# Optimization experiments

Hardware: AMD Instinct MI355X
Metric: run time of the kernel (lower is better)

## Reference

```python
import jax, jax.numpy as jnp
import numpy as np

B, P, D = 128, 32, 256
DIST_THD = 1.5


def setup_inputs() -> dict:
    key = jax.random.key(0)
    ks = jax.random.split(key, 16)
    s2d = 1.0 / np.sqrt(2 * D)
    s1d = 1.0 / np.sqrt(D)
    return {
        "fea_data": jax.random.normal(ks[0], (B, P, D), jnp.float32),
        "pos_data": jax.random.normal(ks[1], (B, P, 2), jnp.float32),
        # pair_encoder: Linear(2D->D), ReLU, (Dropout=id), Linear(D->D); weights stored [in,out]
        "pe_w1": jax.random.normal(ks[2], (2 * D, D), jnp.float32) * s2d,
        "pe_b1": jax.random.normal(ks[3], (D,), jnp.float32) * s2d,
        "pe_w2": jax.random.normal(ks[4], (D, D), jnp.float32) * s1d,
        "pe_b2": jax.random.normal(ks[5], (D,), jnp.float32) * s1d,
        # spatial_mixer: same structure
        "sm_w1": jax.random.normal(ks[6], (2 * D, D), jnp.float32) * s2d,
        "sm_b1": jax.random.normal(ks[7], (D,), jnp.float32) * s2d,
        "sm_w2": jax.random.normal(ks[8], (D, D), jnp.float32) * s1d,
        "sm_b2": jax.random.normal(ks[9], (D,), jnp.float32) * s1d,
        "diff_wts": jax.random.normal(ks[10], (P, D), jnp.float32),
        "diff_bias": jax.random.normal(ks[11], (P,), jnp.float32),
        "gconv_wt": jax.random.normal(ks[12], (2 * D, D), jnp.float32),
    }


def reference(fea_data, pos_data, pe_w1, pe_b1, pe_w2, pe_b2,
              sm_w1, sm_b1, sm_w2, sm_b2, diff_wts, diff_bias, gconv_wt):
    dtype = fea_data.dtype
    # --- spatial_interact ---
    # pair_encoder(cat(x_p1, x_p2)): split W1 into the x_p1 and x_p2 halves so the
    # [B,P,P,2D] concat is never materialized.
    a = fea_data @ pe_w1[:D]          # [B,P,D] contribution of p1
    c = fea_data @ pe_w1[D:]          # [B,P,D] contribution of p2
    h = jax.nn.relu(a[:, :, None, :] + c[:, None, :, :] + pe_b1)  # [B,P,P,D]
    # sum over p2 of (h @ W2 + b2) == (sum h) @ W2 + P*b2 (linear)
    interact_sum = h.sum(axis=2) @ pe_w2 + P * pe_b2              # [B,P,D]
    mix_in = jnp.concatenate([fea_data, interact_sum], axis=-1)   # [B,P,2D]
    spatial = jax.nn.relu(mix_in @ sm_w1 + sm_b1) @ sm_w2 + sm_b2 # [B,P,D]
    # --- residual_diffs ---
    logits = fea_data @ diff_wts.T + diff_bias                    # [B,P(p1),P(p2)]
    w = jax.nn.softmax(logits, axis=-1)
    # sum_p2 w*(x_p1 - x_p2) = x_p1 - w @ x   (softmax weights sum to 1)
    diff = fea_data - jnp.einsum('bpq,bqd->bpd', w, fea_data)     # [B,P,D]
    merged = jnp.concatenate([spatial, diff], axis=-1)            # [B,P,2D]
    # --- neighbor_mat ---
    dist = jnp.linalg.norm(pos_data[:, :, None, :] - pos_data[:, None, :, :], axis=-1)
    off_diag = ~jnp.eye(P, dtype=bool)
    adj = ((dist < DIST_THD) & off_diag).astype(dtype)            # [B,P,P]
    # --- sync_gconv ---
    adj = adj + jnp.eye(P, dtype=dtype)
    deg = adj.sum(axis=2, keepdims=True) + 1e-6                   # [B,P,1]
    dinv = deg ** -0.5
    norm_adj = dinv * adj * jnp.swapaxes(dinv, 1, 2)
    out = jnp.einsum('bpq,bqf->bpf', norm_adj, merged) @ gconv_wt # [B,P,D]
    return jax.nn.relu(out)
```

## Files before the change

### kernel.cpp

```cpp
#include <hip/hip_runtime.h>
#include <math.h>

#define Dk 256
#define Pk 32
#define Bk 128

using f32x4    = __attribute__((ext_vector_type(4))) float;
using short8   = __attribute__((ext_vector_type(8))) short;
using short4v  = __attribute__((ext_vector_type(4))) short;
using ushort4v = __attribute__((ext_vector_type(4))) unsigned short;

static __device__ __forceinline__ unsigned short bf16_rtne(float x) {
    unsigned u = __float_as_uint(x);
    return (unsigned short)((u + 0x7fffu + ((u >> 16) & 1u)) >> 16);
}
static __device__ __forceinline__ float bf16_back(unsigned short h) {
    return __uint_as_float(((unsigned)h) << 16);
}
static __device__ __forceinline__ void split2(float x, unsigned short& h, unsigned short& l) {
    h = bf16_rtne(x);
    l = bf16_rtne(x - bf16_back(h));
}

__device__ __forceinline__ void gemm_core(
    const unsigned short* __restrict__ AH, const unsigned short* __restrict__ AL, int lda,
    const unsigned short* __restrict__ BloH, const unsigned short* __restrict__ BloL,
    const unsigned short* __restrict__ BhiH, const unsigned short* __restrict__ BhiL,
    int splitK, int K, int row0, int col0,
    short (*Ah)[72], short (*Al)[72], short (*Bh)[72], short (*Bl)[72],
    f32x4 acc[2][2])
{
    const int tid  = threadIdx.x;
    const int l    = tid & 63;
    const int w    = tid >> 6;
    const int wm   = w >> 1, wn = w & 1;
    const int role = l & 15, g = l >> 4;
    const int sr   = tid >> 3;
    const int scg  = (tid & 7) * 8;

    short8 pAH[2], pAL[2], pBH[2], pBL[2];
    auto prefetch = [&](int k0) {
        const unsigned short *bH, *bL; int kk;
        if (k0 < splitK) { bH = BloH; bL = BloL; kk = k0; }
        else             { bH = BhiH; bL = BhiL; kk = k0 - splitK; }
        #pragma unroll
        for (int it = 0; it < 2; ++it) {
            int r = sr + it * 32;
            pAH[it] = *(const short8*)(AH + (size_t)(row0 + r) * lda + k0 + scg);
            pAL[it] = *(const short8*)(AL + (size_t)(row0 + r) * lda + k0 + scg);
            pBH[it] = *(const short8*)(bH + (size_t)(col0 + r) * 256 + kk + scg);
            pBL[it] = *(const short8*)(bL + (size_t)(col0 + r) * 256 + kk + scg);
        }
    };

    prefetch(0);
    const int nk = K >> 6;
    for (int kt = 0; kt < nk; ++kt) {
        #pragma unroll
        for (int it = 0; it < 2; ++it) {
            int r = sr + it * 32;
            *(short8*)&Ah[r][scg] = pAH[it];
            *(short8*)&Al[r][scg] = pAL[it];
            *(short8*)&Bh[r][scg] = pBH[it];
            *(short8*)&Bl[r][scg] = pBL[it];
        }
        __syncthreads();
        if (kt + 1 < nk) prefetch((kt + 1) << 6);
        #pragma unroll
        for (int ks = 0; ks < 2; ++ks) {
            short8 fah[2], fal[2], fbh[2], fbl[2];
            #pragma unroll
            for (int mt = 0; mt < 2; ++mt) {
                int r = wm * 32 + mt * 16 + role, c = ks * 32 + g * 8;
                fah[mt] = *(const short8*)&Ah[r][c];
                fal[mt] = *(const short8*)&Al[r][c];
            }
            #pragma unroll
            for (int nt = 0; nt < 2; ++nt) {
                int r = wn * 32 + nt * 16 + role, c = ks * 32 + g * 8;
                fbh[nt] = *(const short8*)&Bh[r][c];
                fbl[nt] = *(const short8*)&Bl[r][c];
            }
            #pragma unroll
            for (int mt = 0; mt < 2; ++mt)
                #pragma unroll
                for (int nt = 0; nt < 2; ++nt) {
                    acc[mt][nt] = __builtin_amdgcn_mfma_f32_16x16x32_bf16(fah[mt], fbh[nt], acc[mt][nt], 0, 0, 0);
                    acc[mt][nt] = __builtin_amdgcn_mfma_f32_16x16x32_bf16(fah[mt], fbl[nt], acc[mt][nt], 0, 0, 0);
                    acc[mt][nt] = __builtin_amdgcn_mfma_f32_16x16x32_bf16(fal[mt], fbh[nt], acc[mt][nt], 0, 0, 0);
                }
        }
        __syncthreads();
    }
}

__global__ __launch_bounds__(256)
void prep_kernel(const float* __restrict__ fea, const float* __restrict__ pe_w1,
                 const float* __restrict__ pe_w2, const float* __restrict__ pe_b2,
                 const float* __restrict__ sm_w1, const float* __restrict__ sm_b1,
                 const float* __restrict__ sm_w2, const float* __restrict__ sm_b2,
                 const float* __restrict__ gconv,
                 const float* __restrict__ diff_wts, const float* __restrict__ diff_bias,
                 unsigned short* __restrict__ MIX2H, unsigned short* __restrict__ MIX2L,
                 unsigned short* __restrict__ WpTH,  unsigned short* __restrict__ WpTL,
                 unsigned short* __restrict__ SW1TH, unsigned short* __restrict__ SW1TL,
                 unsigned short* __restrict__ GBTH,  unsigned short* __restrict__ GBTL,
                 unsigned short* __restrict__ W1pTH, unsigned short* __restrict__ W1pTL,
                 unsigned short* __restrict__ W2pTH, unsigned short* __restrict__ W2pTL,
                 float* __restrict__ b1p, float* __restrict__ b2p,
                 unsigned short* __restrict__ CATH, unsigned short* __restrict__ CATL)
{
    __shared__ __align__(16) char smbuf[70272];
    const int blk = blockIdx.x;
    const int tid = threadIdx.x;

    if (blk < 256) {
        int r0 = blk * 16;
        #pragma unroll
        for (int i = 0; i < 4; ++i) {
            int q  = tid + i * 256;
            int r  = r0 + (q >> 6);
            int c4 = (q & 63) * 4;
            f32x4 v = *(const f32x4*)(fea + (size_t)r * 256 + c4);
            ushort4v h, lo;
            #pragma unroll
            for (int j = 0; j < 4; ++j) { unsigned short hh, ll; split2(v[j], hh, ll); h[j] = hh; lo[j] = ll; }
            *(ushort4v*)&MIX2H[(size_t)r * 512 + c4] = h;
            *(ushort4v*)&MIX2L[(size_t)r * 512 + c4] = lo;
        }
    } else if (blk < 320) {
        int t  = blk - 256;
        int grp = t >> 4, tt = t & 15;
        int tr = tt >> 2, tc = tt & 3;
        const float* src; unsigned short *dH, *dL; int ilv, ofs;
        if (grp == 0)      { src = pe_w1;         dH = WpTH;  dL = WpTL;  ilv = 1; ofs = 0; }
        else if (grp == 1) { src = pe_w1 + 65536; dH = WpTH;  dL = WpTL;  ilv = 1; ofs = 1; }
        else if (grp == 2) { src = sm_w1;         dH = SW1TH; dL = SW1TL; ilv = 0; ofs = 0; }
        else               { src = gconv + 65536; dH = GBTH;  dL = GBTL;  ilv = 0; ofs = 0; }
        float (*ts)[65] = (float (*)[65])smbuf;
        #pragma unroll
        for (int i = 0; i < 4; ++i) {
            int q = tid + i * 256;
            int r = q >> 4, c4 = (q & 15) * 4;
            f32x4 v = *(const f32x4*)(src + (size_t)(tr * 64 + r) * 256 + tc * 64 + c4);
            ts[r][c4 + 0] = v[0]; ts[r][c4 + 1] = v[1]; ts[r][c4 + 2] = v[2]; ts[r][c4 + 3] = v[3];
        }
        __syncthreads();
        #pragma unroll
        for (int i = 0; i < 4; ++i) {
            int q = tid + i * 256;
            int n = q >> 4, k4 = (q & 15) * 4;
            ushort4v h, lo;
            #pragma unroll
            for (int j = 0; j < 4; ++j) { unsigned short hh, ll; split2(ts[k4 + j][n], hh, ll); h[j] = hh; lo[j] = ll; }
            int srcN   = tc * 64 + n;
            int dstRow = ilv ? (2 * srcN + ofs) : srcN;
            *(ushort4v*)&dH[(size_t)dstRow * 256 + tr * 64 + k4] = h;
            *(ushort4v*)&dL[(size_t)dstRow * 256 + tr * 64 + k4] = lo;
        }
    } else if (blk < 322) {
        int j = tid;
        if (blk == 320) {
            float s = 0.f;
            for (int k = 0; k < 256; ++k) s = fmaf(pe_b2[k], sm_w1[(size_t)(256 + k) * 256 + j], s);
            b1p[j] = s * (float)Pk + sm_b1[j];
        } else {
            float s = 0.f;
            for (int k = 0; k < 256; ++k) s = fmaf(sm_b2[k], gconv[(size_t)k * 256 + j], s);
            b2p[j] = s;
        }
    } else if (blk < 354) {
        int u = blk - 322;
        int z = u >> 4, tt = u & 15;
        int row0 = (tt >> 2) * 64, col0 = (tt & 3) * 64;
        const float* Af; const float* Bf; unsigned short *dH, *dL;
        if (z == 0) { Af = pe_w2; Bf = sm_w1 + 65536; dH = W1pTH; dL = W1pTL; }
        else        { Af = sm_w2; Bf = gconv;         dH = W2pTH; dL = W2pTL; }
        short (*Ah)[72] = (short (*)[72])(smbuf);
        short (*Al)[72] = (short (*)[72])(smbuf + 9216);
        short (*Bh)[72] = (short (*)[72])(smbuf + 18432);
        short (*Bl)[72] = (short (*)[72])(smbuf + 27648);
        const int l = tid & 63, w = tid >> 6, wm = w >> 1, wn = w & 1, role = l & 15, g = l >> 4;
        const int ar = tid >> 2, ac = (tid & 3) << 4;
        const int bc = (tid & 15) << 2, bk = (tid >> 4) << 2;
        f32x4 acc[2][2];
        #pragma unroll
        for (int i = 0; i < 2; ++i)
            #pragma unroll
            for (int j = 0; j < 2; ++j) acc[i][j] = (f32x4){0.f, 0.f, 0.f, 0.f};
        f32x4 aPf[4], bPf[4];
        auto load_tile = [&](int k0) {
            const float* Ap = Af + (size_t)(row0 + ar) * 256 + k0 + ac;
            #pragma unroll
            for (int j = 0; j < 4; ++j) aPf[j] = *(const f32x4*)(Ap + j * 4);
            #pragma unroll
            for (int jj = 0; jj < 4; ++jj)
                bPf[jj] = *(const f32x4*)(Bf + (size_t)(k0 + bk + jj) * 256 + col0 + bc);
        };
        load_tile(0);
        for (int kt = 0; kt < 4; ++kt) {
            {
                short8 h0, h1, l0, l1;
                #pragma unroll
                for (int j = 0; j < 4; ++j)
                    #pragma unroll
                    for (int e = 0; e < 4; ++e) {
                        unsigned short hh, ll; split2(aPf[j][e], hh, ll);
                        int idx = j * 4 + e;
                        if (idx < 8) { h0[idx] = (short)hh; l0[idx] = (short)ll; }
                        else         { h1[idx - 8] = (short)hh; l1[idx - 8] = (short)ll; }
                    }
                *(short8*)&Ah[ar][ac] = h0; *(short8*)&Ah[ar][ac + 8] = h1;
                *(short8*)&Al[ar][ac] = l0; *(short8*)&Al[ar][ac + 8] = l1;
                #pragma unroll
                for (int j = 0; j < 4; ++j) {
                    short4v h4, l4;
                    #pragma unroll
                    for (int jj = 0; jj < 4; ++jj) {
                        unsigned short hh, ll; split2(bPf[jj][j], hh, ll);
                        h4[jj] = (short)hh; l4[jj] = (short)ll;
                    }
                    *(short4v*)&Bh[bc + j][bk] = h4;
                    *(short4v*)&Bl[bc + j][bk] = l4;
                }
            }
            __syncthreads();
            if (kt + 1 < 4) load_tile((kt + 1) << 6);
            #pragma unroll
            for (int ks = 0; ks < 2; ++ks) {
                short8 fah[2], fal[2], fbh[2], fbl[2];
                #pragma unroll
                for (int mt = 0; mt < 2; ++mt) {
                    int r = wm * 32 + mt * 16 + role, c = ks * 32 + g * 8;
                    fah[mt] = *(const short8*)&Ah[r][c];
                    fal[mt] = *(const short8*)&Al[r][c];
                }
                #pragma unroll
                for (int nt = 0; nt < 2; ++nt) {
                    int r = wn * 32 + nt * 16 + role, c = ks * 32 + g * 8;
                    fbh[nt] = *(const short8*)&Bh[r][c];
                    fbl[nt] = *(const short8*)&Bl[r][c];
                }
                #pragma unroll
                for (int mt = 0; mt < 2; ++mt)
                    #pragma unroll
                    for (int nt = 0; nt < 2; ++nt) {
                        acc[mt][nt] = __builtin_amdgcn_mfma_f32_16x16x32_bf16(fah[mt], fbh[nt], acc[mt][nt], 0, 0, 0);
                        acc[mt][nt] = __builtin_amdgcn_mfma_f32_16x16x32_bf16(fah[mt], fbl[nt], acc[mt][nt], 0, 0, 0);
                        acc[mt][nt] = __builtin_amdgcn_mfma_f32_16x16x32_bf16(fal[mt], fbh[nt], acc[mt][nt], 0, 0, 0);
                    }
            }
            __syncthreads();
        }
        #pragma unroll
        for (int mt = 0; mt < 2; ++mt)
            #pragma unroll
            for (int nt = 0; nt < 2; ++nt) {
                int col = col0 + wn * 32 + nt * 16 + role;
                #pragma unroll
                for (int r = 0; r < 4; ++r) {
                    int row = row0 + wm * 32 + mt * 16 + g * 4 + r;
                    unsigned short hh, ll; split2(acc[mt][nt][r], hh, ll);
                    dH[(size_t)col * 256 + row] = hh;
                    dL[(size_t)col * 256 + row] = ll;
                }
            }
    } else {
        int b = blk - 354;
        float (*fs)[260] = (float (*)[260])(smbuf);
        float (*dwT)[32] = (float (*)[32])(smbuf + 33280);
        float (*wm_)[33] = (float (*)[33])(smbuf + 66048);
        const float* fb = fea + (size_t)b * 8192;
        #pragma unroll
        for (int i = 0; i < 8; ++i) {
            int q = tid + i * 256;
            int r = q >> 6, c4 = (q & 63) << 2;
            f32x4 v = *(const f32x4*)(fb + r * 256 + c4);
            fs[r][c4 + 0] = v[0]; fs[r][c4 + 1] = v[1]; fs[r][c4 + 2] = v[2]; fs[r][c4 + 3] = v[3];
        }
        {
            int p2 = tid & 31, kq = tid >> 5;
            #pragma unroll
            for (int i = 0; i < 8; ++i) {
                int c4 = ((kq << 3) + i) << 2;
                f32x4 v = *(const f32x4*)(diff_wts + (size_t)p2 * 256 + c4);
                dwT[c4 + 0][p2] = v[0]; dwT[c4 + 1][p2] = v[1];
                dwT[c4 + 2][p2] = v[2]; dwT[c4 + 3][p2] = v[3];
            }
        }
        __syncthreads();
        {
            const int p1 = tid >> 3, p2b = (tid & 7) << 2;
            f32x4 s = {0.f, 0.f, 0.f, 0.f};
            for (int k4 = 0; k4 < 256; k4 += 4) {
                f32x4 fv = *(const f32x4*)&fs[p1][k4];
                #pragma unroll
                for (int e = 0; e < 4; ++e) {
                    f32x4 dv = *(const f32x4*)&dwT[k4 + e][p2b];
                    s[0] = fmaf(fv[e], dv[0], s[0]);
                    s[1] = fmaf(fv[e], dv[1], s[1]);
                    s[2] = fmaf(fv[e], dv[2], s[2]);
                    s[3] = fmaf(fv[e], dv[3], s[3]);
                }
            }
            #pragma unroll
            for (int j = 0; j < 4; ++j) wm_[p1][p2b + j] = s[j] + diff_bias[p2b + j];
        }
        __syncthreads();
        if (tid < 32) {
            float m = wm_[tid][0];
            #pragma unroll
            for (int j = 1; j < 32; ++j) m = fmaxf(m, wm_[tid][j]);
            float e[32]; float sum = 0.f;
            #pragma unroll
            for (int j = 0; j < 32; ++j) { e[j] = __expf(wm_[tid][j] - m); sum += e[j]; }
            float inv = 1.f / sum;
            #pragma unroll
            for (int j = 0; j < 32; ++j) wm_[tid][j] = e[j] * inv;
        }
        __syncthreads();
        float fv[32];
        #pragma unroll
        for (int p2 = 0; p2 < 32; ++p2) fv[p2] = fs[p2][tid];
        for (int p1 = 0; p1 < 32; ++p1) {
            float s = 0.f;
            #pragma unroll
            for (int p2 = 0; p2 < 32; ++p2) s = fmaf(wm_[p1][p2], fv[p2], s);
            float v = fv[p1] - s;
            unsigned short hh, ll; split2(v, hh, ll);
            size_t o = (size_t)(b * 32 + p1) * 512 + 256 + tid;
            CATH[o] = hh; CATL[o] = ll;
        }
    }
}

__global__ __launch_bounds__(256)
void g1_hsum(const unsigned short* __restrict__ MIX2H, const unsigned short* __restrict__ MIX2L,
             const unsigned short* __restrict__ WpTH, const unsigned short* __restrict__ WpTL,
             const float* __restrict__ pe_b1,
             unsigned short* __restrict__ MH, unsigned short* __restrict__ ML)
{
    __shared__ __align__(16) char smbuf[36864];
    short (*Ah)[72] = (short (*)[72])(smbuf);
    short (*Al)[72] = (short (*)[72])(smbuf + 9216);
    short (*Bh)[72] = (short (*)[72])(smbuf + 18432);
    short (*Bl)[72] = (short (*)[72])(smbuf + 27648);
    const int row0 = blockIdx.y * 64, col0 = blockIdx.x * 64;
    f32x4 acc[2][2];
    #pragma unroll
    for (int i = 0; i < 2; ++i)
        #pragma unroll
        for (int j = 0; j < 2; ++j) acc[i][j] = (f32x4){0.f, 0.f, 0.f, 0.f};

    gemm_core(MIX2H, MIX2L, 512, WpTH, WpTL, nullptr, nullptr, 1 << 30, 256,
              row0, col0, Ah, Al, Bh, Bl, acc);

    float (*ms)[68] = (float (*)[68])(smbuf);
    const int tid = threadIdx.x;
    const int l = tid & 63, w = tid >> 6, wm = w >> 1, wn = w & 1, role = l & 15, g = l >> 4;
    #pragma unroll
    for (int mt = 0; mt < 2; ++mt)
        #pragma unroll
        for (int nt = 0; nt < 2; ++nt)
            #pragma unroll
            for (int r = 0; r < 4; ++r)
                ms[wm * 32 + mt * 16 + g * 4 + r][wn * 32 + nt * 16 + role] = acc[mt][nt][r];
    __syncthreads();

    const int dd = tid & 31, bloc = (tid >> 5) & 1, pg = tid >> 6;
    const float b1v = pe_b1[blockIdx.x * 32 + dd];
    float apre[8], sum[8];
    #pragma unroll
    for (int i = 0; i < 8; ++i) {
        apre[i] = ms[bloc * 32 + pg * 8 + i][2 * dd] + b1v;
        sum[i] = 0.f;
    }
    for (int p2 = 0; p2 < 32; ++p2) {
        float cv = ms[bloc * 32 + p2][2 * dd + 1];
        #pragma unroll
        for (int i = 0; i < 8; ++i) sum[i] += fmaxf(apre[i] + cv, 0.f);
    }
    const int colg = 256 + blockIdx.x * 32 + dd;
    #pragma unroll
    for (int i = 0; i < 8; ++i) {
        int rowg = (2 * blockIdx.y + bloc) * 32 + pg * 8 + i;
        unsigned short hh, ll; split2(sum[i], hh, ll);
        MH[(size_t)rowg * 512 + colg] = hh;
        ML[(size_t)rowg * 512 + colg] = ll;
    }
}

__global__ __launch_bounds__(256)
void g3_kernel(const unsigned short* __restrict__ MIX2H, const unsigned short* __restrict__ MIX2L,
               const unsigned short* __restrict__ SW1TH, const unsigned short* __restrict__ SW1TL,
               const unsigned short* __restrict__ W1pTH, const unsigned short* __restrict__ W1pTL,
               const float* __restrict__ b1p,
               unsigned short* __restrict__ CATH, unsigned short* __restrict__ CATL)
{
    __shared__ __align__(16) char smbuf[36864];
    short (*Ah)[72] = (short (*)[72])(smbuf);
    short (*Al)[72] = (short (*)[72])(smbuf + 9216);
    short (*Bh)[72] = (short (*)[72])(smbuf + 18432);
    short (*Bl)[72] = (short (*)[72])(smbuf + 27648);
    const int row0 = blockIdx.y * 64, col0 = blockIdx.x * 64;
    f32x4 acc[2][2];
    #pragma unroll
    for (int i = 0; i < 2; ++i)
        #pragma unroll
        for (int j = 0; j < 2; ++j) acc[i][j] = (f32x4){0.f, 0.f, 0.f, 0.f};

    gemm_core(MIX2H, MIX2L, 512, SW1TH, SW1TL, W1pTH, W1pTL, 256, 512,
              row0, col0, Ah, Al, Bh, Bl, acc);

    const int tid = threadIdx.x;
    const int l = tid & 63, w = tid >> 6, wm = w >> 1, wn = w & 1, role = l & 15, g = l >> 4;
    float bv[2];
    #pragma unroll
    for (int nt = 0; nt < 2; ++nt) bv[nt] = b1p[col0 + wn * 32 + nt * 16 + role];
    #pragma unroll
    for (int mt = 0; mt < 2; ++mt)
        #pragma unroll
        for (int nt = 0; nt < 2; ++nt) {
            int col = col0 + wn * 32 + nt * 16 + role;
            #pragma unroll
            for (int r = 0; r < 4; ++r) {
                int row = row0 + wm * 32 + mt * 16 + g * 4 + r;
                float v = fmaxf(acc[mt][nt][r] + bv[nt], 0.f);
                unsigned short hh, ll; split2(v, hh, ll);
                CATH[(size_t)row * 512 + col] = hh;
                CATL[(size_t)row * 512 + col] = ll;
            }
        }
}

__global__ __launch_bounds__(256)
void g5_adj(const unsigned short* __restrict__ CATH, const unsigned short* __restrict__ CATL,
            const unsigned short* __restrict__ W2pTH, const unsigned short* __restrict__ W2pTL,
            const unsigned short* __restrict__ GBTH, const unsigned short* __restrict__ GBTL,
            const float* __restrict__ b2p, const float* __restrict__ pos,
            float* __restrict__ out)
{
    __shared__ __align__(16) char smbuf[44032];
    short (*Ah)[72] = (short (*)[72])(smbuf);
    short (*Al)[72] = (short (*)[72])(smbuf + 9216);
    short (*Bh)[72] = (short (*)[72])(smbuf + 18432);
    short (*Bl)[72] = (short (*)[72])(smbuf + 27648);
    const int row0 = blockIdx.y * 64, col0 = blockIdx.x * 64;
    f32x4 acc[2][2];
    #pragma unroll
    for (int i = 0; i < 2; ++i)
        #pragma unroll
        for (int j = 0; j < 2; ++j) acc[i][j] = (f32x4){0.f, 0.f, 0.f, 0.f};

    gemm_core(CATH, CATL, 512, W2pTH, W2pTL, GBTH, GBTL, 256, 512,
              row0, col0, Ah, Al, Bh, Bl, acc);

    float (*ms)[68]  = (float (*)[68])(smbuf);
    float* px        = (float*)(smbuf + 17408);
    float* py        = (float*)(smbuf + 17664);
    float* dinv_     = (float*)(smbuf + 17920);
    float (*na)[33]  = (float (*)[33])(smbuf + 18176);
    float (*ot)[68]  = (float (*)[68])(smbuf + 26624);

    const int tid = threadIdx.x;
    const int l = tid & 63, w = tid >> 6, wm = w >> 1, wn = w & 1, role = l & 15, g = l >> 4;
    float bv[2];
    #pragma unroll
    for (int nt = 0; nt < 2; ++nt) bv[nt] = b2p[col0 + wn * 32 + nt * 16 + role];
    #pragma unroll
    for (int mt = 0; mt < 2; ++mt)
        #pragma unroll
        for (int nt = 0; nt < 2; ++nt)
            #pragma unroll
            for (int r = 0; r < 4; ++r)
                ms[wm * 32 + mt * 16 + g * 4 + r][wn * 32 + nt * 16 + role] = acc[mt][nt][r] + bv[nt];

    const int b0 = 2 * blockIdx.y;
    if (tid < 64) {
        int bi = tid >> 5, pp = tid & 31;
        px[bi * 32 + pp] = pos[(size_t)(b0 + bi) * 64 + pp * 2 + 0];
        py[bi * 32 + pp] = pos[(size_t)(b0 + bi) * 64 + pp * 2 + 1];
    }
    __syncthreads();
    {
        int bi = tid >> 7, p1 = (tid >> 2) & 31, p2g = (tid & 3) * 8;
        #pragma unroll
        for (int j = 0; j < 8; ++j) {
            int p2 = p2g + j;
            float v;
            if (p1 == p2) v = 1.f;
            else {
                float dx = px[bi * 32 + p1] - px[bi * 32 + p2];
                float dy = py[bi * 32 + p1] - py[bi * 32 + p2];
                v = (sqrtf(dx * dx + dy * dy) < 1.5f) ? 1.f : 0.f;
            }
            na[bi * 32 + p1][p2] = v;
        }
    }
    __syncthreads();
    if (tid < 64) {
        int r = tid;
        float s = 0.f;
        #pragma unroll
        for (int j = 0; j < 32; ++j) s += na[r][j];
        dinv_[r] = 1.f / sqrtf(s + 1e-6f);
    }
    __syncthreads();
    {
        int bi = tid >> 7, p1 = (tid >> 2) & 31, p2g = (tid & 3) * 8;
        #pragma unroll
        for (int j = 0; j < 8; ++j) {
            int p2 = p2g + j;
            na[bi * 32 + p1][p2] *= dinv_[bi * 32 + p1] * dinv_[bi * 32 + p2];
        }
    }
    __syncthreads();
    {
        const int p1 = tid & 31, bi = (tid >> 5) & 1, fg = (tid >> 6) * 16;
        f32x4 s4[4];
        #pragma unroll
        for (int j = 0; j < 4; ++j) s4[j] = (f32x4){0.f, 0.f, 0.f, 0.f};
        for (int p2 = 0; p2 < 32; ++p2) {
            float nv = na[bi * 32 + p1][p2];
            const f32x4* mrow = (const f32x4*)&ms[bi * 32 + p2][fg];
            #pragma unroll
            for (int j = 0; j < 4; ++j) {
                f32x4 mv = mrow[j];
                s4[j][0] = fmaf(nv, mv[0], s4[j][0]);
                s4[j][1] = fmaf(nv, mv[1], s4[j][1]);
                s4[j][2] = fmaf(nv, mv[2], s4[j][2]);
                s4[j][3] = fmaf(nv, mv[3], s4[j][3]);
            }
        }
        #pragma unroll
        for (int j = 0; j < 4; ++j)
            #pragma unroll
            for (int e = 0; e < 4; ++e)
                ot[bi * 32 + p1][fg + j * 4 + e] = s4[j][e];
    }
    __syncthreads();
    #pragma unroll
    for (int i = 0; i < 16; ++i) {
        int q = tid + i * 256;
        int row = q >> 6, f = q & 63;
        out[(size_t)(b0 * 32 + row) * 256 + col0 + f] = fmaxf(ot[row][f], 0.f);
    }
}

extern "C" void kernel_launch(void* const* d_in, const int* in_sizes, int n_in,
                              void* d_out, int out_size, void* d_ws, size_t ws_size,
                              hipStream_t stream)
{
    const float* fea       = (const float*)d_in[0];
    const float* pos       = (const float*)d_in[1];
    const float* pe_w1     = (const float*)d_in[2];
    const float* pe_b1     = (const float*)d_in[3];
    const float* pe_w2     = (const float*)d_in[4];
    const float* pe_b2     = (const float*)d_in[5];
    const float* sm_w1     = (const float*)d_in[6];
    const float* sm_b1     = (const float*)d_in[7];
    const float* sm_w2     = (const float*)d_in[8];
    const float* sm_b2     = (const float*)d_in[9];
    const float* diff_wts  = (const float*)d_in[10];
    const float* diff_bias = (const float*)d_in[11];
    const float* gconv     = (const float*)d_in[12];
    float* out = (float*)d_out;
    char*  ws  = (char*)d_ws;

    unsigned short* MIX2H = (unsigned short*)(ws + 0);
    unsigned short* MIX2L = (unsigned short*)(ws + 4194304);
    unsigned short* CATH  = (unsigned short*)(ws + 8388608);
    unsigned short* CATL  = (unsigned short*)(ws + 12582912);
    unsigned short* WpTH  = (unsigned short*)(ws + 16777216);
    unsigned short* WpTL  = (unsigned short*)(ws + 17039360);
    unsigned short* SW1TH = (unsigned short*)(ws + 17301504);
    unsigned short* SW1TL = (unsigned short*)(ws + 17432576);
    unsigned short* GBTH  = (unsigned short*)(ws + 17563648);
    unsigned short* GBTL  = (unsigned short*)(ws + 17694720);
    unsigned short* W1pTH = (unsigned short*)(ws + 17825792);
    unsigned short* W1pTL = (unsigned short*)(ws + 17956864);
    unsigned short* W2pTH = (unsigned short*)(ws + 18087936);
    unsigned short* W2pTL = (unsigned short*)(ws + 18219008);
    float*          b1p   = (float*)(ws + 18350080);
    float*          b2p   = (float*)(ws + 18351104);

    prep_kernel<<<482, 256, 0, stream>>>(fea, pe_w1, pe_w2, pe_b2, sm_w1, sm_b1,
                                         sm_w2, sm_b2, gconv, diff_wts, diff_bias,
                                         MIX2H, MIX2L, WpTH, WpTL, SW1TH, SW1TL,
                                         GBTH, GBTL, W1pTH, W1pTL, W2pTH, W2pTL,
                                         b1p, b2p, CATH, CATL);
    g1_hsum<<<dim3(8, 64), 256, 0, stream>>>(MIX2H, MIX2L, WpTH, WpTL, pe_b1, MIX2H, MIX2L);
    g3_kernel<<<dim3(4, 64), 256, 0, stream>>>(MIX2H, MIX2L, SW1TH, SW1TL, W1pTH, W1pTL,
                                               b1p, CATH, CATL);
    g5_adj<<<dim3(4, 64), 256, 0, stream>>>(CATH, CATL, W2pTH, W2pTL, GBTH, GBTL,
                                            b2p, pos, out);
}
```

Baseline: 128.6 us.

## Merge four kernel launches into one cooperative persistent kernel with grid syncs

Turns the prep, g1, g3 and g5 kernels into device functions and calls them from a single cooperative kernel of 256 blocks, with grid.sync() between stages. Blocks loop over the 482 prep roles and the 512 g1 tiles. The aim is to remove the launch gaps and per-kernel tail costs between the four stages. The trade-off is fewer blocks, which lowers parallelism for prep and g1, a larger shared-memory footprint for every stage, and the cost of each grid barrier. If the cooperative launch fails, it falls back to four launches.

```diff
diff --git a/kernel.cpp b/kernel.cpp
--- a/kernel.cpp
+++ b/kernel.cpp
@@ -1,5 +1,8 @@
 #include <hip/hip_runtime.h>
+#include <hip/hip_cooperative_groups.h>
 #include <math.h>
+
+namespace cg = cooperative_groups;
 
 #define Dk 256
 #define Pk 32
@@ -21,6 +24,16 @@
     h = bf16_rtne(x);
     l = bf16_rtne(x - bf16_back(h));
 }
+
+struct Args {
+    const float *fea, *pos, *pe_w1, *pe_b1, *pe_w2, *pe_b2;
+    const float *sm_w1, *sm_b1, *sm_w2, *sm_b2, *diff_wts, *diff_bias, *gconv;
+    unsigned short *MIX2H, *MIX2L, *WpTH, *WpTL, *SW1TH, *SW1TL, *GBTH, *GBTL;
+    unsigned short *W1pTH, *W1pTL, *W2pTH, *W2pTL;
+    float *b1p, *b2p;
+    unsigned short *CATH, *CATL;
+    float *out;
+};
 
 __device__ __forceinline__ void gemm_core(
     const unsigned short* __restrict__ AH, const unsigned short* __restrict__ AL, int lda,
@@ -94,26 +107,8 @@
     }
 }
 
-__global__ __launch_bounds__(256)
-void prep_kernel(const float* __restrict__ fea, const float* __restrict__ pe_w1,
-                 const float* __restrict__ pe_w2, const float* __restrict__ pe_b2,
-                 const float* __restrict__ sm_w1, const float* __restrict__ sm_b1,
-                 const float* __restrict__ sm_w2, const float* __restrict__ sm_b2,
-                 const float* __restrict__ gconv,
-                 const float* __restrict__ diff_wts, const float* __restrict__ diff_bias,
-                 unsigned short* __restrict__ MIX2H, unsigned short* __restrict__ MIX2L,
-                 unsigned short* __restrict__ WpTH,  unsigned short* __restrict__ WpTL,
-                 unsigned short* __restrict__ SW1TH, unsigned short* __restrict__ SW1TL,
-                 unsigned short* __restrict__ GBTH,  unsigned short* __restrict__ GBTL,
-                 unsigned short* __restrict__ W1pTH, unsigned short* __restrict__ W1pTL,
-                 unsigned short* __restrict__ W2pTH, unsigned short* __restrict__ W2pTL,
-                 float* __restrict__ b1p, float* __restrict__ b2p,
-                 unsigned short* __restrict__ CATH, unsigned short* __restrict__ CATL)
+__device__ __forceinline__ void do_role(const Args& A, char* smbuf, int blk, int tid)
 {
-    __shared__ __align__(16) char smbuf[70272];
-    const int blk = blockIdx.x;
-    const int tid = threadIdx.x;
-
     if (blk < 256) {
         int r0 = blk * 16;
         #pragma unroll
@@ -121,22 +116,22 @@
             int q  = tid + i * 256;
             int r  = r0 + (q >> 6);
             int c4 = (q & 63) * 4;
-            f32x4 v = *(const f32x4*)(fea + (size_t)r * 256 + c4);
+            f32x4 v = *(const f32x4*)(A.fea + (size_t)r * 256 + c4);
             ushort4v h, lo;
             #pragma unroll
             for (int j = 0; j < 4; ++j) { unsigned short hh, ll; split2(v[j], hh, ll); h[j] = hh; lo[j] = ll; }
-            *(ushort4v*)&MIX2H[(size_t)r * 512 + c4] = h;
-            *(ushort4v*)&MIX2L[(size_t)r * 512 + c4] = lo;
+            *(ushort4v*)&A.MIX2H[(size_t)r * 512 + c4] = h;
+            *(ushort4v*)&A.MIX2L[(size_t)r * 512 + c4] = lo;
         }
     } else if (blk < 320) {
         int t  = blk - 256;
         int grp = t >> 4, tt = t & 15;
         int tr = tt >> 2, tc = tt & 3;
         const float* src; unsigned short *dH, *dL; int ilv, ofs;
-        if (grp == 0)      { src = pe_w1;         dH = WpTH;  dL = WpTL;  ilv = 1; ofs = 0; }
-        else if (grp == 1) { src = pe_w1 + 65536; dH = WpTH;  dL = WpTL;  ilv = 1; ofs = 1; }
-        else if (grp == 2) { src = sm_w1;         dH = SW1TH; dL = SW1TL; ilv = 0; ofs = 0; }
-        else               { src = gconv + 65536; dH = GBTH;  dL = GBTL;  ilv = 0; ofs = 0; }
+        if (grp == 0)      { src = A.pe_w1;         dH = A.WpTH;  dL = A.WpTL;  ilv = 1; ofs = 0; }
+        else if (grp == 1) { src = A.pe_w1 + 65536; dH = A.WpTH;  dL = A.WpTL;  ilv = 1; ofs = 1; }
+        else if (grp == 2) { src = A.sm_w1;         dH = A.SW1TH; dL = A.SW1TL; ilv = 0; ofs = 0; }
+        else               { src = A.gconv + 65536; dH = A.GBTH;  dL = A.GBTL;  ilv = 0; ofs = 0; }
         float (*ts)[65] = (float (*)[65])smbuf;
         #pragma unroll
         for (int i = 0; i < 4; ++i) {
@@ -162,20 +157,20 @@
         int j = tid;
         if (blk == 320) {
             float s = 0.f;
-            for (int k = 0; k < 256; ++k) s = fmaf(pe_b2[k], sm_w1[(size_t)(256 + k) * 256 + j], s);
-            b1p[j] = s * (float)Pk + sm_b1[j];
+            for (int k = 0; k < 256; ++k) s = fmaf(A.pe_b2[k], A.sm_w1[(size_t)(256 + k) * 256 + j], s);
+            A.b1p[j] = s * (float)Pk + A.sm_b1[j];
         } else {
             float s = 0.f;
-            for (int k = 0; k < 256; ++k) s = fmaf(sm_b2[k], gconv[(size_t)k * 256 + j], s);
-            b2p[j] = s;
+            for (int k = 0; k < 256; ++k) s = fmaf(A.sm_b2[k], A.gconv[(size_t)k * 256 + j], s);
+            A.b2p[j] = s;
         }
     } else if (blk < 354) {
         int u = blk - 322;
         int z = u >> 4, tt = u & 15;
         int row0 = (tt >> 2) * 64, col0 = (tt & 3) * 64;
         const float* Af; const float* Bf; unsigned short *dH, *dL;
-        if (z == 0) { Af = pe_w2; Bf = sm_w1 + 65536; dH = W1pTH; dL = W1pTL; }
-        else        { Af = sm_w2; Bf = gconv;         dH = W2pTH; dL = W2pTL; }
+        if (z == 0) { Af = A.pe_w2; Bf = A.sm_w1 + 65536; dH = A.W1pTH; dL = A.W1pTL; }
+        else        { Af = A.sm_w2; Bf = A.gconv;         dH = A.W2pTH; dL = A.W2pTL; }
         short (*Ah)[72] = (short (*)[72])(smbuf);
         short (*Al)[72] = (short (*)[72])(smbuf + 9216);
         short (*Bh)[72] = (short (*)[72])(smbuf + 18432);
@@ -270,7 +265,7 @@
         float (*fs)[260] = (float (*)[260])(smbuf);
         float (*dwT)[32] = (float (*)[32])(smbuf + 33280);
         float (*wm_)[33] = (float (*)[33])(smbuf + 66048);
-        const float* fb = fea + (size_t)b * 8192;
+        const float* fb = A.fea + (size_t)b * 8192;
         #pragma unroll
         for (int i = 0; i < 8; ++i) {
             int q = tid + i * 256;
@@ -283,7 +278,7 @@
             #pragma unroll
             for (int i = 0; i < 8; ++i) {
                 int c4 = ((kq << 3) + i) << 2;
-                f32x4 v = *(const f32x4*)(diff_wts + (size_t)p2 * 256 + c4);
+                f32x4 v = *(const f32x4*)(A.diff_wts + (size_t)p2 * 256 + c4);
                 dwT[c4 + 0][p2] = v[0]; dwT[c4 + 1][p2] = v[1];
                 dwT[c4 + 2][p2] = v[2]; dwT[c4 + 3][p2] = v[3];
             }
@@ -304,7 +299,7 @@
                 }
             }
             #pragma unroll
-            for (int j = 0; j < 4; ++j) wm_[p1][p2b + j] = s[j] + diff_bias[p2b + j];
+            for (int j = 0; j < 4; ++j) wm_[p1][p2b + j] = s[j] + A.diff_bias[p2b + j];
         }
         __syncthreads();
         if (tid < 32) {
@@ -329,34 +324,29 @@
             float v = fv[p1] - s;
             unsigned short hh, ll; split2(v, hh, ll);
             size_t o = (size_t)(b * 32 + p1) * 512 + 256 + tid;
-            CATH[o] = hh; CATL[o] = ll;
-        }
-    }
-}
-
-__global__ __launch_bounds__(256)
-void g1_hsum(const unsigned short* __restrict__ MIX2H, const unsigned short* __restrict__ MIX2L,
-             const unsigned short* __restrict__ WpTH, const unsigned short* __restrict__ WpTL,
-             const float* __restrict__ pe_b1,
-             unsigned short* __restrict__ MH, unsigned short* __restrict__ ML)
+            A.CATH[o] = hh; A.CATL[o] = ll;
+        }
+    }
+}
+
+__device__ __forceinline__ void do_g1(const Args& A, char* smbuf, int t, int tid)
 {
-    __shared__ __align__(16) char smbuf[36864];
+    const int x = t & 7, y = t >> 3;
     short (*Ah)[72] = (short (*)[72])(smbuf);
     short (*Al)[72] = (short (*)[72])(smbuf + 9216);
     short (*Bh)[72] = (short (*)[72])(smbuf + 18432);
     short (*Bl)[72] = (short (*)[72])(smbuf + 27648);
-    const int row0 = blockIdx.y * 64, col0 = blockIdx.x * 64;
+    const int row0 = y * 64, col0 = x * 64;
     f32x4 acc[2][2];
     #pragma unroll
     for (int i = 0; i < 2; ++i)
         #pragma unroll
         for (int j = 0; j < 2; ++j) acc[i][j] = (f32x4){0.f, 0.f, 0.f, 0.f};
 
-    gemm_core(MIX2H, MIX2L, 512, WpTH, WpTL, nullptr, nullptr, 1 << 30, 256,
+    gemm_core(A.MIX2H, A.MIX2L, 512, A.WpTH, A.WpTL, nullptr, nullptr, 1 << 30, 256,
               row0, col0, Ah, Al, Bh, Bl, acc);
 
     float (*ms)[68] = (float (*)[68])(smbuf);
-    const int tid = threadIdx.x;
     const int l = tid & 63, w = tid >> 6, wm = w >> 1, wn = w & 1, role = l & 15, g = l >> 4;
     #pragma unroll
     for (int mt = 0; mt < 2; ++mt)
@@ -368,7 +358,7 @@
     __syncthreads();
 
     const int dd = tid & 31, bloc = (tid >> 5) & 1, pg = tid >> 6;
-    const float b1v = pe_b1[blockIdx.x * 32 + dd];
+    const float b1v = A.pe_b1[x * 32 + dd];
     float apre[8], sum[8];
     #pragma unroll
     for (int i = 0; i < 8; ++i) {
@@ -380,43 +370,37 @@
         #pragma unroll
         for (int i = 0; i < 8; ++i) sum[i] += fmaxf(apre[i] + cv, 0.f);
     }
-    const int colg = 256 + blockIdx.x * 32 + dd;
+    const int colg = 256 + x * 32 + dd;
     #pragma unroll
     for (int i = 0; i < 8; ++i) {
-        int rowg = (2 * blockIdx.y + bloc) * 32 + pg * 8 + i;
+        int rowg = (2 * y + bloc) * 32 + pg * 8 + i;
         unsigned short hh, ll; split2(sum[i], hh, ll);
-        MH[(size_t)rowg * 512 + colg] = hh;
-        ML[(size_t)rowg * 512 + colg] = ll;
-    }
-}
-
-__global__ __launch_bounds__(256)
-void g3_kernel(const unsigned short* __restrict__ MIX2H, const unsigned short* __restrict__ MIX2L,
-               const unsigned short* __restrict__ SW1TH, const unsigned short* __restrict__ SW1TL,
-               const unsigned short* __restrict__ W1pTH, const unsigned short* __restrict__ W1pTL,
-               const float* __restrict__ b1p,
-               unsigned short* __restrict__ CATH, unsigned short* __restrict__ CATL)
+        A.MIX2H[(size_t)rowg * 512 + colg] = hh;
+        A.MIX2L[(size_t)rowg * 512 + colg] = ll;
+    }
+}
+
+__device__ __forceinline__ void do_g3(const Args& A, char* smbuf, int t, int tid)
 {
-    __shared__ __align__(16) char smbuf[36864];
+    const int x = t & 3, y = t >> 2;
     short (*Ah)[72] = (short (*)[72])(smbuf);
     short (*Al)[72] = (short (*)[72])(smbuf + 9216);
     short (*Bh)[72] = (short (*)[72])(smbuf + 18432);
     short (*Bl)[72] = (short (*)[72])(smbuf + 27648);
-    const int row0 = blockIdx.y * 64, col0 = blockIdx.x * 64;
+    const int row0 = y * 64, col0 = x * 64;
     f32x4 acc[2][2];
     #pragma unroll
     for (int i = 0; i < 2; ++i)
         #pragma unroll
         for (int j = 0; j < 2; ++j) acc[i][j] = (f32x4){0.f, 0.f, 0.f, 0.f};
 
-    gemm_core(MIX2H, MIX2L, 512, SW1TH, SW1TL, W1pTH, W1pTL, 256, 512,
+    gemm_core(A.MIX2H, A.MIX2L, 512, A.SW1TH, A.SW1TL, A.W1pTH, A.W1pTL, 256, 512,
               row0, col0, Ah, Al, Bh, Bl, acc);
 
-    const int tid = threadIdx.x;
     const int l = tid & 63, w = tid >> 6, wm = w >> 1, wn = w & 1, role = l & 15, g = l >> 4;
     float bv[2];
     #pragma unroll
-    for (int nt = 0; nt < 2; ++nt) bv[nt] = b1p[col0 + wn * 32 + nt * 16 + role];
+    for (int nt = 0; nt < 2; ++nt) bv[nt] = A.b1p[col0 + wn * 32 + nt * 16 + role];
     #pragma unroll
     for (int mt = 0; mt < 2; ++mt)
         #pragma unroll
@@ -427,32 +411,27 @@
                 int row = row0 + wm * 32 + mt * 16 + g * 4 + r;
                 float v = fmaxf(acc[mt][nt][r] + bv[nt], 0.f);
                 unsigned short hh, ll; split2(v, hh, ll);
-                CATH[(size_t)row * 512 + col] = hh;
-                CATL[(size_t)row * 512 + col] = ll;
-            }
-        }
-}
-
-__global__ __launch_bounds__(256)
-void g5_adj(const unsigned short* __restrict__ CATH, const unsigned short* __restrict__ CATL,
-            const unsigned short* __restrict__ W2pTH, const unsigned short* __restrict__ W2pTL,
-            const unsigned short* __restrict__ GBTH, const unsigned short* __restrict__ GBTL,
-            const float* __restrict__ b2p, const float* __restrict__ pos,
-            float* __restrict__ out)
+                A.CATH[(size_t)row * 512 + col] = hh;
+                A.CATL[(size_t)row * 512 + col] = ll;
+            }
+        }
+}
+
+__device__ __forceinline__ void do_g5(const Args& A, char* smbuf, int t, int tid)
 {
-    __shared__ __align__(16) char smbuf[44032];
+    const int x = t & 3, y = t >> 2;
     short (*Ah)[72] = (short (*)[72])(smbuf);
     short (*Al)[72] = (short (*)[72])(smbuf + 9216);
     short (*Bh)[72] = (short (*)[72])(smbuf + 18432);
     short (*Bl)[72] = (short (*)[72])(smbuf + 27648);
-    const int row0 = blockIdx.y * 64, col0 = blockIdx.x * 64;
+    const int row0 = y * 64, col0 = x * 64;
     f32x4 acc[2][2];
     #pragma unroll
     for (int i = 0; i < 2; ++i)
         #pragma unroll
         for (int j = 0; j < 2; ++j) acc[i][j] = (f32x4){0.f, 0.f, 0.f, 0.f};
 
-    gemm_core(CATH, CATL, 512, W2pTH, W2pTL, GBTH, GBTL, 256, 512,
+    gemm_core(A.CATH, A.CATL, 512, A.W2pTH, A.W2pTL, A.GBTH, A.GBTL, 256, 512,
               row0, col0, Ah, Al, Bh, Bl, acc);
 
     float (*ms)[68]  = (float (*)[68])(smbuf);
@@ -462,11 +441,10 @@
     float (*na)[33]  = (float (*)[33])(smbuf + 18176);
     float (*ot)[68]  = (float (*)[68])(smbuf + 26624);
 
-    const int tid = threadIdx.x;
     const int l = tid & 63, w = tid >> 6, wm = w >> 1, wn = w & 1, role = l & 15, g = l >> 4;
     float bv[2];
     #pragma unroll
-    for (int nt = 0; nt < 2; ++nt) bv[nt] = b2p[col0 + wn * 32 + nt * 16 + role];
+    for (int nt = 0; nt < 2; ++nt) bv[nt] = A.b2p[col0 + wn * 32 + nt * 16 + role];
     #pragma unroll
     for (int mt = 0; mt < 2; ++mt)
         #pragma unroll
@@ -475,11 +453,11 @@
             for (int r = 0; r < 4; ++r)
                 ms[wm * 32 + mt * 16 + g * 4 + r][wn * 32 + nt * 16 + role] = acc[mt][nt][r] + bv[nt];
 
-    const int b0 = 2 * blockIdx.y;
+    const int b0 = 2 * y;
     if (tid < 64) {
         int bi = tid >> 5, pp = tid & 31;
-        px[bi * 32 + pp] = pos[(size_t)(b0 + bi) * 64 + pp * 2 + 0];
-        py[bi * 32 + pp] = pos[(size_t)(b0 + bi) * 64 + pp * 2 + 1];
+        px[bi * 32 + pp] = A.pos[(size_t)(b0 + bi) * 64 + pp * 2 + 0];
+        py[bi * 32 + pp] = A.pos[(size_t)(b0 + bi) * 64 + pp * 2 + 1];
     }
     __syncthreads();
     {
@@ -499,11 +477,10 @@
     }
     __syncthreads();
     if (tid < 64) {
-        int r = tid;
         float s = 0.f;
         #pragma unroll
-        for (int j = 0; j < 32; ++j) s += na[r][j];
-        dinv_[r] = 1.f / sqrtf(s + 1e-6f);
+        for (int j = 0; j < 32; ++j) s += na[tid][j];
+        dinv_[tid] = 1.f / sqrtf(s + 1e-6f);
     }
     __syncthreads();
     {
@@ -543,7 +520,44 @@
     for (int i = 0; i < 16; ++i) {
         int q = tid + i * 256;
         int row = q >> 6, f = q & 63;
-        out[(size_t)(b0 * 32 + row) * 256 + col0 + f] = fmaxf(ot[row][f], 0.f);
+        A.out[(size_t)(b0 * 32 + row) * 256 + col0 + f] = fmaxf(ot[row][f], 0.f);
+    }
+}
+
+__global__ __launch_bounds__(256, 2)
+void mega_kernel(Args A, int mode)
+{
+    __shared__ __align__(16) char smbuf[70272];
+    const int bid = blockIdx.x;
+    const int tid = threadIdx.x;
+
+    if (mode < 0) {
+        cg::grid_group grid = cg::this_grid();
+        for (int r = bid; r < 482; r += 256) {
+            if (r != bid) __syncthreads();
+            do_role(A, smbuf, r, tid);
+        }
+        grid.sync();
+        do_g1(A, smbuf, bid, tid);
+        __syncthreads();
+        do_g1(A, smbuf, bid + 256, tid);
+        grid.sync();
+        do_g3(A, smbuf, bid, tid);
+        grid.sync();
+        do_g5(A, smbuf, bid, tid);
+    } else if (mode == 0) {
+        for (int r = bid; r < 482; r += 256) {
+            if (r != bid) __syncthreads();
+            do_role(A, smbuf, r, tid);
+        }
+    } else if (mode == 1) {
+        do_g1(A, smbuf, bid, tid);
+        __syncthreads();
+        do_g1(A, smbuf, bid + 256, tid);
+    } else if (mode == 2) {
+        do_g3(A, smbuf, bid, tid);
+    } else {
+        do_g5(A, smbuf, bid, tid);
     }
 }
 
@@ -551,47 +565,50 @@
                               void* d_out, int out_size, void* d_ws, size_t ws_size,
                               hipStream_t stream)
 {
-    const float* fea       = (const float*)d_in[0];
-    const float* pos       = (const float*)d_in[1];
-    const float* pe_w1     = (const float*)d_in[2];
-    const float* pe_b1     = (const float*)d_in[3];
-    const float* pe_w2     = (const float*)d_in[4];
-    const float* pe_b2     = (const float*)d_in[5];
-    const float* sm_w1     = (const float*)d_in[6];
-    const float* sm_b1     = (const float*)d_in[7];
-    const float* sm_w2     = (const float*)d_in[8];
-    const float* sm_b2     = (const float*)d_in[9];
-    const float* diff_wts  = (const float*)d_in[10];
-    const float* diff_bias = (const float*)d_in[11];
-    const float* gconv     = (const float*)d_in[12];
-    float* out = (float*)d_out;
-    char*  ws  = (char*)d_ws;
-
-    unsigned short* MIX2H = (unsigned short*)(ws + 0);
-    unsigned short* MIX2L = (unsigned short*)(ws + 4194304);
-    unsigned short* CATH  = (unsigned short*)(ws + 8388608);
-    unsigned short* CATL  = (unsigned short*)(ws + 12582912);
-    unsigned short* WpTH  = (unsigned short*)(ws + 16777216);
-    unsigned short* WpTL  = (unsigned short*)(ws + 17039360);
-    unsigned short* SW1TH = (unsigned short*)(ws + 17301504);
-    unsigned short* SW1TL = (unsigned short*)(ws + 17432576);
-    unsigned short* GBTH  = (unsigned short*)(ws + 17563648);
-    unsigned short* GBTL  = (unsigned short*)(ws + 17694720);
-    unsigned short* W1pTH = (unsigned short*)(ws + 17825792);
-    unsigned short* W1pTL = (unsigned short*)(ws + 17956864);
-    unsigned short* W2pTH = (unsigned short*)(ws + 18087936);
-    unsigned short* W2pTL = (unsigned short*)(ws + 18219008);
-    float*          b1p   = (float*)(ws + 18350080);
-    float*          b2p   = (float*)(ws + 18351104);
-
-    prep_kernel<<<482, 256, 0, stream>>>(fea, pe_w1, pe_w2, pe_b2, sm_w1, sm_b1,
-                                         sm_w2, sm_b2, gconv, diff_wts, diff_bias,
-                                         MIX2H, MIX2L, WpTH, WpTL, SW1TH, SW1TL,
-                                         GBTH, GBTL, W1pTH, W1pTL, W2pTH, W2pTL,
-                                         b1p, b2p, CATH, CATL);
-    g1_hsum<<<dim3(8, 64), 256, 0, stream>>>(MIX2H, MIX2L, WpTH, WpTL, pe_b1, MIX2H, MIX2L);
-    g3_kernel<<<dim3(4, 64), 256, 0, stream>>>(MIX2H, MIX2L, SW1TH, SW1TL, W1pTH, W1pTL,
-                                               b1p, CATH, CATL);
-    g5_adj<<<dim3(4, 64), 256, 0, stream>>>(CATH, CATL, W2pTH, W2pTL, GBTH, GBTL,
-                                            b2p, pos, out);
-}
+    char* ws = (char*)d_ws;
+
+    Args a;
+    a.fea       = (const float*)d_in[0];
+    a.pos       = (const float*)d_in[1];
+    a.pe_w1     = (const float*)d_in[2];
+    a.pe_b1     = (const float*)d_in[3];
+    a.pe_w2     = (const float*)d_in[4];
+    a.pe_b2     = (const float*)d_in[5];
+    a.sm_w1     = (const float*)d_in[6];
+    a.sm_b1     = (const float*)d_in[7];
+    a.sm_w2     = (const float*)d_in[8];
+    a.sm_b2     = (const float*)d_in[9];
+    a.diff_wts  = (const float*)d_in[10];
+    a.diff_bias = (const float*)d_in[11];
+    a.gconv     = (const float*)d_in[12];
+    a.out       = (float*)d_out;
+
+    a.MIX2H = (unsigned short*)(ws + 0);
+    a.MIX2L = (unsigned short*)(ws + 4194304);
+    a.CATH  = (unsigned short*)(ws + 8388608);
+    a.CATL  = (unsigned short*)(ws + 12582912);
+    a.WpTH  = (unsigned short*)(ws + 16777216);
+    a.WpTL  = (unsigned short*)(ws + 17039360);
+    a.SW1TH = (unsigned short*)(ws + 17301504);
+    a.SW1TL = (unsigned short*)(ws + 17432576);
+    a.GBTH  = (unsigned short*)(ws + 17563648);
+    a.GBTL  = (unsigned short*)(ws + 17694720);
+    a.W1pTH = (unsigned short*)(ws + 17825792);
+    a.W1pTL = (unsigned short*)(ws + 17956864);
+    a.W2pTH = (unsigned short*)(ws + 18087936);
+    a.W2pTL = (unsigned short*)(ws + 18219008);
+    a.b1p   = (float*)(ws + 18350080);
+    a.b2p   = (float*)(ws + 18351104);
+
+    int mode = -1;
+    void* kargs[] = { (void*)&a, (void*)&mode };
+    hipError_t e = hipLaunchCooperativeKernel((const void*)mega_kernel,
+                                              dim3(256), dim3(256), kargs, 0, stream);
+    if (e != hipSuccess) {
+        (void)hipGetLastError();
+        mega_kernel<<<256, 256, 0, stream>>>(a, 0);
+        mega_kernel<<<256, 256, 0, stream>>>(a, 1);
+        mega_kernel<<<256, 256, 0, stream>>>(a, 2);
+        mega_kernel<<<256, 256, 0, stream>>>(a, 3);
+    }
+}
```

New measurement: 246.5 us. 1.92x slower.
